# Kernel optimization log

Measured on AMD Instinct MI355X. Metric: run time of the kernel, lower is better.

## Reference

```python
import jax, jax.numpy as jnp
import numpy as np


def setup_inputs() -> dict:
    key = jax.random.key(0)
    k1, k2 = jax.random.split(key)
    p1 = jax.random.normal(k1, (4, 8192, 3), dtype=jnp.float32)
    p2 = jax.random.normal(k2, (4, 8192, 3), dtype=jnp.float32)
    return {"p1": p1, "p2": p2}


def reference(p1, p2):
    # dist[b, n, m] = ||p1[b, n] - p2[b, m]||^2  (faithful to broadcasted diff)
    diff = p1[:, :, None, :] - p2[:, None, :, :]          # [B, N, M, 3]
    dist = jnp.sum(diff * diff, axis=-1)                  # [B, N, M]
    p1_to_p2 = jnp.min(dist, axis=-1)                     # [B, N]
    p2_to_p1 = jnp.min(dist, axis=-2)                     # [B, M]
    chamfer = (p1_to_p2.mean(axis=-1) + p2_to_p1.mean(axis=-1)).mean()
    return chamfer
```

## Files before the change

### kernel.cpp

```cpp
#include <hip/hip_runtime.h>

#define THREADS 256
#define QPT 16
#define SLICES 64
#define NPTS 8192
#define BATCH 4
#define SLICE (NPTS / SLICES)
#define NMINS (2 * BATCH * NPTS)

typedef float f4 __attribute__((ext_vector_type(4)));


__global__ void chamfer_init(unsigned int* mins, float* out) {
    int i = blockIdx.x * blockDim.x + threadIdx.x;
    mins[i] = 0x7F800000u;
    if (i == 0) out[0] = 0.0f;
}

__global__ __launch_bounds__(THREADS, 4) void chamfer_main(
    const float* __restrict__ p1, const float* __restrict__ p2,
    unsigned int* __restrict__ mins)
{
    const int tid  = threadIdx.x;
    const int bz   = blockIdx.z;
    const int dir  = bz >> 2;
    const int b    = bz & 3;
    const int qbase = blockIdx.x * (THREADS * QPT);
    const int tbase = blockIdx.y * SLICE;

    const float* __restrict__ qsrc = (dir == 0) ? p1 : p2;
    const float* __restrict__ tsrc = (dir == 0) ? p2 : p1;

    __shared__ f4 tgt[SLICE];
    {
        const float* tp = tsrc + ((size_t)b * NPTS + tbase) * 3;
        for (int k = tid; k < SLICE; k += THREADS) {
            float x = tp[k * 3 + 0];
            float y = tp[k * 3 + 1];
            float z = tp[k * 3 + 2];
            tgt[k] = f4{-2.0f * x, -2.0f * y, -2.0f * z,
                        fmaf(x, x, fmaf(y, y, z * z))};
        }
    }

    float qx[QPT], qy[QPT], qz[QPT], best[QPT];
#pragma unroll
    for (int j = 0; j < QPT; ++j) {
        const int q = qbase + j * THREADS + tid;
        const float* pq = qsrc + ((size_t)b * NPTS + q) * 3;
        qx[j] = pq[0];
        qy[j] = pq[1];
        qz[j] = pq[2];
        best[j] = 3.0e38f;
    }

    __syncthreads();

#pragma unroll 2
    for (int m = 0; m < SLICE; m += 2) {
        f4 ta = tgt[m];
        f4 tb = tgt[m + 1];
#pragma unroll
        for (int j = 0; j < QPT; ++j) {
            float da = fmaf(qz[j], ta.z, ta.w);
            da = fmaf(qy[j], ta.y, da);
            da = fmaf(qx[j], ta.x, da);
            float db = fmaf(qz[j], tb.z, tb.w);
            db = fmaf(qy[j], tb.y, db);
            db = fmaf(qx[j], tb.x, db);
            best[j] = fminf(fminf(best[j], da), db);
        }
    }

    unsigned int* mbase = mins + ((size_t)dir * BATCH + b) * NPTS;
#pragma unroll
    for (int j = 0; j < QPT; ++j) {
        float q2 = fmaf(qx[j], qx[j], fmaf(qy[j], qy[j], qz[j] * qz[j]));
        float v = fmaxf(best[j] + q2, 0.0f);
        atomicMin(&mbase[qbase + j * THREADS + tid], __float_as_uint(v));
    }
}

__global__ __launch_bounds__(THREADS) void chamfer_reduce(
    const uint4* __restrict__ mins, float* __restrict__ out)
{
    const int i = blockIdx.x * THREADS + threadIdx.x;
    uint4 u = mins[i];
    float s = __uint_as_float(u.x) + __uint_as_float(u.y)
            + __uint_as_float(u.z) + __uint_as_float(u.w);
#pragma unroll
    for (int off = 32; off >= 1; off >>= 1)
        s += __shfl_down(s, off, 64);
    __shared__ float partial[THREADS / 64];
    if ((threadIdx.x & 63) == 0) partial[threadIdx.x >> 6] = s;
    __syncthreads();
    if (threadIdx.x == 0) {
        float tot = 0.0f;
#pragma unroll
        for (int w = 0; w < THREADS / 64; ++w) tot += partial[w];
        atomicAdd(out, tot * (1.0f / (BATCH * NPTS)));
    }
}

extern "C" void kernel_launch(void* const* d_in, const int* in_sizes, int n_in,
                              void* d_out, int out_size, void* d_ws, size_t ws_size,
                              hipStream_t stream) {
    const float* p1 = (const float*)d_in[0];
    const float* p2 = (const float*)d_in[1];
    unsigned int* mins = (unsigned int*)d_ws;
    float* out = (float*)d_out;

    chamfer_init<<<NMINS / THREADS, THREADS, 0, stream>>>(mins, out);

    dim3 grid(NPTS / (THREADS * QPT), SLICES, 2 * BATCH);
    chamfer_main<<<grid, THREADS, 0, stream>>>(p1, p2, mins);

    chamfer_reduce<<<NMINS / (4 * THREADS), THREADS, 0, stream>>>(
        (const uint4*)mins, out);
}
```

Before: 97.85 us.

## Compute each pairwise distance once for both chamfer directions

Replaces the two-direction brute-force pass with one symmetric kernel. Each p1–p2 distance now updates the row minimum in registers and the column minimum through wave shuffles plus LDS atomicMin. Per-slice row partials and per-tile column partials go to workspace, and a finish kernel reduces them and accumulates the mean, which also drops the init kernel. The cost is extra shuffles per target pair and a 16MB partial buffer to read back; the old path is kept as a fallback when the workspace is too small.

Result: slower. 201.7 us (+106.2%).

```diff
diff --git a/kernel.cpp b/kernel.cpp
--- a/kernel.cpp
+++ b/kernel.cpp
@@ -2,64 +2,57 @@
 
 #define THREADS 256
 #define QPT 16
-#define SLICES 64
 #define NPTS 8192
 #define BATCH 4
-#define SLICE (NPTS / SLICES)
-#define NMINS (2 * BATCH * NPTS)
+#define SLICE 64
+#define SLICES (NPTS / SLICE)
+#define XTILES (NPTS / (THREADS * QPT))
+#define NROWS (BATCH * NPTS)
 
 typedef float f4 __attribute__((ext_vector_type(4)));
 
-
-__global__ void chamfer_init(unsigned int* mins, float* out) {
-    int i = blockIdx.x * blockDim.x + threadIdx.x;
-    mins[i] = 0x7F800000u;
-    if (i == 0) out[0] = 0.0f;
-}
-
-__global__ __launch_bounds__(THREADS, 4) void chamfer_main(
+#define ROWPART_FLOATS ((size_t)BATCH * SLICES * NPTS)
+#define COLPART_FLOATS ((size_t)BATCH * XTILES * NPTS)
+#define WS_NEEDED ((ROWPART_FLOATS + COLPART_FLOATS) * 4)
+
+__global__ __launch_bounds__(THREADS, 4) void chamfer_sym(
     const float* __restrict__ p1, const float* __restrict__ p2,
-    unsigned int* __restrict__ mins)
-{
-    const int tid  = threadIdx.x;
-    const int bz   = blockIdx.z;
-    const int dir  = bz >> 2;
-    const int b    = bz & 3;
-    const int qbase = blockIdx.x * (THREADS * QPT);
-    const int tbase = blockIdx.y * SLICE;
-
-    const float* __restrict__ qsrc = (dir == 0) ? p1 : p2;
-    const float* __restrict__ tsrc = (dir == 0) ? p2 : p1;
+    float* __restrict__ rowpart, float* __restrict__ colpart,
+    float* __restrict__ out)
+{
+    const int tid = threadIdx.x;
+    const int bx  = blockIdx.x;
+    const int by  = blockIdx.y;
+    const int b   = blockIdx.z;
+    const int qbase = bx * (THREADS * QPT);
+    const int tbase = by * SLICE;
 
     __shared__ f4 tgt[SLICE];
-    {
-        const float* tp = tsrc + ((size_t)b * NPTS + tbase) * 3;
-        for (int k = tid; k < SLICE; k += THREADS) {
-            float x = tp[k * 3 + 0];
-            float y = tp[k * 3 + 1];
-            float z = tp[k * 3 + 2];
-            tgt[k] = f4{-2.0f * x, -2.0f * y, -2.0f * z,
-                        fmaf(x, x, fmaf(y, y, z * z))};
-        }
-    }
-
-    float qx[QPT], qy[QPT], qz[QPT], best[QPT];
+    __shared__ unsigned int cmin[SLICE];
+    if (tid < SLICE) {
+        const float* tp = p2 + ((size_t)b * NPTS + tbase + tid) * 3;
+        float x = tp[0], y = tp[1], z = tp[2];
+        tgt[tid] = f4{-2.0f * x, -2.0f * y, -2.0f * z,
+                      fmaf(x, x, fmaf(y, y, z * z))};
+        cmin[tid] = 0x7F800000u;
+    }
+
+    float qx[QPT], qy[QPT], qz[QPT], q2[QPT], best[QPT];
 #pragma unroll
     for (int j = 0; j < QPT; ++j) {
         const int q = qbase + j * THREADS + tid;
-        const float* pq = qsrc + ((size_t)b * NPTS + q) * 3;
-        qx[j] = pq[0];
-        qy[j] = pq[1];
-        qz[j] = pq[2];
+        const float* pq = p1 + ((size_t)b * NPTS + q) * 3;
+        qx[j] = pq[0]; qy[j] = pq[1]; qz[j] = pq[2];
+        q2[j] = fmaf(qx[j], qx[j], fmaf(qy[j], qy[j], qz[j] * qz[j]));
         best[j] = 3.0e38f;
     }
-
     __syncthreads();
 
 #pragma unroll 2
     for (int m = 0; m < SLICE; m += 2) {
         f4 ta = tgt[m];
         f4 tb = tgt[m + 1];
+        float ca = 3.0e38f, cb = 3.0e38f;
 #pragma unroll
         for (int j = 0; j < QPT; ++j) {
             float da = fmaf(qz[j], ta.z, ta.w);
@@ -69,12 +62,125 @@
             db = fmaf(qy[j], tb.y, db);
             db = fmaf(qx[j], tb.x, db);
             best[j] = fminf(fminf(best[j], da), db);
-        }
-    }
-
+            ca = fminf(ca, da + q2[j]);
+            cb = fminf(cb, db + q2[j]);
+        }
+#pragma unroll
+        for (int off = 1; off < 64; off <<= 1) {
+            ca = fminf(ca, __shfl_xor(ca, off, 64));
+            cb = fminf(cb, __shfl_xor(cb, off, 64));
+        }
+        if ((tid & 63) == 0) {
+            atomicMin(&cmin[m],     __float_as_uint(fmaxf(ca, 0.0f)));
+            atomicMin(&cmin[m + 1], __float_as_uint(fmaxf(cb, 0.0f)));
+        }
+    }
+    __syncthreads();
+
+    float* rp = rowpart + ((size_t)(b * SLICES + by)) * NPTS;
+#pragma unroll
+    for (int j = 0; j < QPT; ++j) {
+        float v = fmaxf(best[j] + q2[j], 0.0f);
+        rp[qbase + j * THREADS + tid] = v;
+    }
+    if (tid < SLICE)
+        colpart[((size_t)(b * XTILES + bx)) * NPTS + tbase + tid] =
+            __uint_as_float(cmin[tid]);
+
+    if (bx == 0 && by == 0 && b == 0 && tid == 0)
+        out[0] = 0.0f;
+}
+
+__global__ __launch_bounds__(THREADS) void chamfer_finish(
+    const float* __restrict__ rowpart, const float* __restrict__ colpart,
+    float* __restrict__ out)
+{
+    const int tid = threadIdx.x;
+    const int gid = blockIdx.x * THREADS + tid;
+    const int b   = gid >> 13;
+    const int r   = gid & (NPTS - 1);
+
+    float m = 3.0e38f;
+    const float* rb = rowpart + (size_t)b * SLICES * NPTS + r;
+#pragma unroll 8
+    for (int y = 0; y < SLICES; ++y)
+        m = fminf(m, rb[(size_t)y * NPTS]);
+
+    const float* cb = colpart + (size_t)b * XTILES * NPTS + r;
+    float c = fminf(cb[0], cb[(size_t)NPTS]);
+
+    float s = m + c;
+#pragma unroll
+    for (int off = 1; off < 64; off <<= 1)
+        s += __shfl_xor(s, off, 64);
+    __shared__ float part[THREADS / 64];
+    if ((tid & 63) == 0) part[tid >> 6] = s;
+    __syncthreads();
+    if (tid == 0) {
+        float tot = part[0] + part[1] + part[2] + part[3];
+        atomicAdd(out, tot * (1.0f / (BATCH * NPTS)));
+    }
+}
+
+#define NMINS (2 * BATCH * NPTS)
+#define FB_QPT 16
+#define FB_SLICES 64
+#define FB_SLICE (NPTS / FB_SLICES)
+
+__global__ void chamfer_init(unsigned int* mins, float* out) {
+    int i = blockIdx.x * blockDim.x + threadIdx.x;
+    mins[i] = 0x7F800000u;
+    if (i == 0) out[0] = 0.0f;
+}
+
+__global__ __launch_bounds__(THREADS, 4) void chamfer_brute(
+    const float* __restrict__ p1, const float* __restrict__ p2,
+    unsigned int* __restrict__ mins)
+{
+    const int tid  = threadIdx.x;
+    const int bz   = blockIdx.z;
+    const int dir  = bz >> 2;
+    const int b    = bz & 3;
+    const int qbase = blockIdx.x * (THREADS * FB_QPT);
+    const int tbase = blockIdx.y * FB_SLICE;
+    const float* __restrict__ qsrc = (dir == 0) ? p1 : p2;
+    const float* __restrict__ tsrc = (dir == 0) ? p2 : p1;
+
+    __shared__ f4 tgt[FB_SLICE];
+    {
+        const float* tp = tsrc + ((size_t)b * NPTS + tbase) * 3;
+        for (int k = tid; k < FB_SLICE; k += THREADS) {
+            float x = tp[k * 3 + 0], y = tp[k * 3 + 1], z = tp[k * 3 + 2];
+            tgt[k] = f4{-2.0f * x, -2.0f * y, -2.0f * z,
+                        fmaf(x, x, fmaf(y, y, z * z))};
+        }
+    }
+    float qx[FB_QPT], qy[FB_QPT], qz[FB_QPT], best[FB_QPT];
+#pragma unroll
+    for (int j = 0; j < FB_QPT; ++j) {
+        const int q = qbase + j * THREADS + tid;
+        const float* pq = qsrc + ((size_t)b * NPTS + q) * 3;
+        qx[j] = pq[0]; qy[j] = pq[1]; qz[j] = pq[2];
+        best[j] = 3.0e38f;
+    }
+    __syncthreads();
+#pragma unroll 2
+    for (int m = 0; m < FB_SLICE; m += 2) {
+        f4 ta = tgt[m], tb = tgt[m + 1];
+#pragma unroll
+        for (int j = 0; j < FB_QPT; ++j) {
+            float da = fmaf(qz[j], ta.z, ta.w);
+            da = fmaf(qy[j], ta.y, da);
+            da = fmaf(qx[j], ta.x, da);
+            float db = fmaf(qz[j], tb.z, tb.w);
+            db = fmaf(qy[j], tb.y, db);
+            db = fmaf(qx[j], tb.x, db);
+            best[j] = fminf(fminf(best[j], da), db);
+        }
+    }
     unsigned int* mbase = mins + ((size_t)dir * BATCH + b) * NPTS;
 #pragma unroll
-    for (int j = 0; j < QPT; ++j) {
+    for (int j = 0; j < FB_QPT; ++j) {
         float q2 = fmaf(qx[j], qx[j], fmaf(qy[j], qy[j], qz[j] * qz[j]));
         float v = fmaxf(best[j] + q2, 0.0f);
         atomicMin(&mbase[qbase + j * THREADS + tid], __float_as_uint(v));
@@ -107,14 +213,22 @@
                               hipStream_t stream) {
     const float* p1 = (const float*)d_in[0];
     const float* p2 = (const float*)d_in[1];
-    unsigned int* mins = (unsigned int*)d_ws;
     float* out = (float*)d_out;
 
-    chamfer_init<<<NMINS / THREADS, THREADS, 0, stream>>>(mins, out);
-
-    dim3 grid(NPTS / (THREADS * QPT), SLICES, 2 * BATCH);
-    chamfer_main<<<grid, THREADS, 0, stream>>>(p1, p2, mins);
-
-    chamfer_reduce<<<NMINS / (4 * THREADS), THREADS, 0, stream>>>(
-        (const uint4*)mins, out);
-}
+    if (ws_size >= WS_NEEDED) {
+        float* rowpart = (float*)d_ws;
+        float* colpart = rowpart + ROWPART_FLOATS;
+
+        dim3 grid(XTILES, SLICES, BATCH);
+        chamfer_sym<<<grid, THREADS, 0, stream>>>(p1, p2, rowpart, colpart, out);
+
+        chamfer_finish<<<NROWS / THREADS, THREADS, 0, stream>>>(rowpart, colpart, out);
+    } else {
+        unsigned int* mins = (unsigned int*)d_ws;
+        chamfer_init<<<NMINS / THREADS, THREADS, 0, stream>>>(mins, out);
+        dim3 grid(NPTS / (THREADS * FB_QPT), FB_SLICES, 2 * BATCH);
+        chamfer_brute<<<grid, THREADS, 0, stream>>>(p1, p2, mins);
+        chamfer_reduce<<<NMINS / (4 * THREADS), THREADS, 0, stream>>>(
+            (const uint4*)mins, out);
+    }
+}
```
